# Optimization experiments

Hardware: AMD Instinct MI355X
Metric: run time of the kernel (lower is better)

Reference implementation:

```python
import jax, jax.numpy as jnp
import numpy as np

EPS = 1e-6


def _rmsnorm(x, w):
    var = jnp.mean(x * x, axis=-1, keepdims=True)
    return x * jax.lax.rsqrt(var + EPS) * w


def _rotate_half(x):
    h = x.shape[-1] // 2
    return jnp.concatenate([-x[..., h:], x[..., :h]], axis=-1)


def setup_inputs() -> dict:
    key = jax.random.key(0)
    B, T, H = 2, 2048, 2048
    nh, nkv, d = 16, 8, 128
    max_pos = 4096
    ks = jax.random.split(key, 6)
    s = 0.02
    x = jax.random.normal(ks[0], (B, T, H), jnp.float32)
    # real RoPE tables (Qwen3 uses rope_theta=1e6)
    inv_freq = 1.0 / (1e6 ** (np.arange(0, d, 2, dtype=np.float64) / d))
    freqs = np.outer(np.arange(max_pos), inv_freq)
    emb = np.concatenate([freqs, freqs], axis=-1)
    cos = jnp.asarray(np.cos(emb), jnp.float32)
    sin = jnp.asarray(np.sin(emb), jnp.float32)
    position_ids = jnp.broadcast_to(jnp.arange(T, dtype=jnp.int32)[None, :], (B, T))
    Wq = jax.random.normal(ks[1], (nh * d, H), jnp.float32) * s
    Wk = jax.random.normal(ks[2], (nkv * d, H), jnp.float32) * s
    Wv = jax.random.normal(ks[3], (nkv * d, H), jnp.float32) * s
    Wo = jax.random.normal(ks[4], (H, nh * d), jnp.float32) * s
    q_norm_w = jnp.ones((d,), jnp.float32)
    k_norm_w = jnp.ones((d,), jnp.float32)
    return {"x": x, "cos": cos, "sin": sin, "position_ids": position_ids,
            "Wq": Wq, "Wk": Wk, "Wv": Wv, "Wo": Wo,
            "q_norm_w": q_norm_w, "k_norm_w": k_norm_w}


def reference(x, cos, sin, position_ids, Wq, Wk, Wv, Wo, q_norm_w, k_norm_w):
    B, T, H = x.shape
    d = q_norm_w.shape[0]
    nh = Wq.shape[0] // d
    nkv = Wk.shape[0] // d
    groups = nh // nkv

    # QKV projections (F.linear: x @ W.T)
    q = jnp.einsum('bth,oh->bto', x, Wq).reshape(B, T, nh, d).transpose(0, 2, 1, 3)   # [B,nh,T,d]
    k = jnp.einsum('bth,oh->bto', x, Wk).reshape(B, T, nkv, d).transpose(0, 2, 1, 3)  # [B,nkv,T,d]
    v = jnp.einsum('bth,oh->bto', x, Wv).reshape(B, T, nkv, d).transpose(0, 2, 1, 3)

    # per-head RMSNorm on q and k
    q = _rmsnorm(q, q_norm_w)
    k = _rmsnorm(k, k_norm_w)

    # RoPE
    cos_b = cos[position_ids][:, None, :, :]  # [B,1,T,d]
    sin_b = sin[position_ids][:, None, :, :]
    q = q * cos_b + _rotate_half(q) * sin_b
    k = k * cos_b + _rotate_half(k) * sin_b

    # GQA expand (repeat_interleave along head dim)
    if groups > 1:
        k = jnp.repeat(k, groups, axis=1)
        v = jnp.repeat(v, groups, axis=1)

    # causal SDPA
    scale = 1.0 / jnp.sqrt(jnp.asarray(d, x.dtype))
    scores = jnp.einsum('bhqd,bhkd->bhqk', q, k) * scale  # [B,nh,T,T]
    causal = jnp.tril(jnp.ones((T, T), bool))
    scores = jnp.where(causal[None, None], scores, jnp.asarray(-jnp.inf, scores.dtype))
    probs = jax.nn.softmax(scores, axis=-1)
    attn = jnp.einsum('bhqk,bhkd->bhqd', probs, v)  # [B,nh,T,d]

    attn = attn.transpose(0, 2, 1, 3).reshape(B, T, nh * d)
    return jnp.einsum('bto,ho->bth', attn, Wo)
```

## Files before the change

kernel.cpp:

```cpp
#include <hip/hip_runtime.h>
#include <stdint.h>
#include <stddef.h>

typedef unsigned short u16;
typedef __attribute__((ext_vector_type(4))) unsigned short u16x4;
typedef __attribute__((ext_vector_type(8))) short bf16x8;
typedef __attribute__((ext_vector_type(4))) float f32x4;
typedef __attribute__((ext_vector_type(16))) float f32x16;

#define B_   2
#define T_   2048
#define NH   16
#define NKV  8
#define HD   128

__device__ __forceinline__ u16 f2bf(float f) {
  union { float f; uint32_t u; } v; v.f = f;
  uint32_t u = v.u;
  u += 0x7FFFu + ((u >> 16) & 1u);
  return (u16)(u >> 16);
}
__device__ __forceinline__ float bf2f(u16 h) {
  union { uint32_t u; float f; } v; v.u = ((uint32_t)h) << 16;
  return v.f;
}
__device__ __forceinline__ uint32_t cvt_pk_bf16(float lo, float hi) {
  uint32_t r;
  asm("v_cvt_pk_bf16_f32 %0, %1, %2" : "=v"(r) : "v"(lo), "v"(hi));
  return r;
}

__device__ __forceinline__ void gload_lds16(const void* g, void* l) {
  __builtin_amdgcn_global_load_lds(
      (__attribute__((address_space(1))) void*)g,
      (__attribute__((address_space(3))) void*)l, 16, 0, 0);
}

__global__ __launch_bounds__(256) void cvt_all(const float* __restrict__ x,
                                               const float* __restrict__ Wq,
                                               const float* __restrict__ Wk,
                                               const float* __restrict__ Wv,
                                               const float* __restrict__ Wo,
                                               u16* __restrict__ ws0) {
  const int blk = blockIdx.x;
  const float* src; u16* dst; int lb;
  if (blk < 8192)       { src = x;  dst = ws0;              lb = blk; }
  else if (blk < 12288) { src = Wq; dst = ws0 +  8388608;   lb = blk - 8192; }
  else if (blk < 14336) { src = Wk; dst = ws0 + 12582912;   lb = blk - 12288; }
  else if (blk < 16384) { src = Wv; dst = ws0 + 14680064;   lb = blk - 14336; }
  else                  { src = Wo; dst = ws0 + 16777216;   lb = blk - 16384; }
  const int i = lb * 256 + threadIdx.x;
  float4 v = reinterpret_cast<const float4*>(src)[i];
  u16x4 o;
  o.x = f2bf(v.x); o.y = f2bf(v.y); o.z = f2bf(v.z); o.w = f2bf(v.w);
  reinterpret_cast<u16x4*>(dst)[i] = o;
}

template<int BM, int BN, int STORE>
__global__ __launch_bounds__(512, 2) void gemm2(const u16* __restrict__ A,
                                                const u16* __restrict__ Bm,
                                                void* __restrict__ C0,
                                                void* __restrict__ C1,
                                                void* __restrict__ C2,
                                                int M, int N, int K) {
  constexpr int FM  = BM / 32;
  constexpr int FN  = BN / 64;
  constexpr int ASZ = BM * 64;
  constexpr int BSZ = BN * 64;
  __shared__ u16 lds[2 * (ASZ + BSZ)];

  const int tid  = threadIdx.x;
  const int lane = tid & 63;
  const int wid  = tid >> 6;
  const int lr   = lane & 15;
  const int lg   = lane >> 4;
  const int wm0 = (wid >> 2) * (BM / 2);
  const int wn0 = (wid & 3) * (BN / 4);

  const int s  = ((blockIdx.x & 7) << 5) | (blockIdx.x >> 3);
  const int nx = N / BN;
  const int m0 = (s / nx) * BM;
  const int n0 = (s % nx) * BN;

  f32x4 acc[FM][FN];
#pragma unroll
  for (int i = 0; i < FM; ++i)
#pragma unroll
    for (int j = 0; j < FN; ++j) acc[i][j] = (f32x4){0.f, 0.f, 0.f, 0.f};

  auto stage = [&](int kt, int p) {
    const int k0 = kt << 6;
    u16* Ab = lds + p * (ASZ + BSZ);
    u16* Bb = Ab + ASZ;
#pragma unroll
    for (int it = 0; it < BM / 64; ++it) {
      const int CI = it * 512 + tid;
      const int row = CI >> 3, c = CI & 7;
      gload_lds16(A + (size_t)(m0 + row) * K + k0 + ((c ^ (row & 7)) << 3),
                  (char*)Ab + (size_t)CI * 16);
    }
#pragma unroll
    for (int it = 0; it < BN / 64; ++it) {
      const int CI = it * 512 + tid;
      const int row = CI >> 3, c = CI & 7;
      gload_lds16(Bm + (size_t)(n0 + row) * K + k0 + ((c ^ (row & 7)) << 3),
                  (char*)Bb + (size_t)CI * 16);
    }
  };

  const int nk = K >> 6;
  stage(0, 0);
  __syncthreads();
  int cur = 0;
  for (int kt = 0; kt < nk; ++kt) {
    if (kt + 1 < nk) stage(kt + 1, cur ^ 1);
    const u16* Ab = lds + cur * (ASZ + BSZ);
    const u16* Bb = Ab + ASZ;
#pragma unroll
    for (int kk = 0; kk < 2; ++kk) {
      bf16x8 af[FM], bfr[FN];
#pragma unroll
      for (int mt = 0; mt < FM; ++mt) {
        const int ar = wm0 + mt * 16 + lr;
        af[mt] = *reinterpret_cast<const bf16x8*>(
            (const char*)Ab + ar * 128 + ((kk * 64 + lg * 16) ^ ((ar & 7) << 4)));
      }
#pragma unroll
      for (int nt = 0; nt < FN; ++nt) {
        const int br = wn0 + nt * 16 + lr;
        bfr[nt] = *reinterpret_cast<const bf16x8*>(
            (const char*)Bb + br * 128 + ((kk * 64 + lg * 16) ^ ((br & 7) << 4)));
      }
      __builtin_amdgcn_s_setprio(1);
#pragma unroll
      for (int mt = 0; mt < FM; ++mt)
#pragma unroll
        for (int nt = 0; nt < FN; ++nt)
          acc[mt][nt] = __builtin_amdgcn_mfma_f32_16x16x32_bf16(
              af[mt], bfr[nt], acc[mt][nt], 0, 0, 0);
      __builtin_amdgcn_s_setprio(0);
    }
    __syncthreads();
    cur ^= 1;
  }

  if (STORE == 3) {
    u16* Qd = (u16*)C0; u16* Kd = (u16*)C1; u16* Vd = (u16*)C2;
    if (n0 < 2048) {
#pragma unroll
      for (int mt = 0; mt < FM; ++mt) {
        const int row = m0 + wm0 + mt * 16 + lg * 4;
#pragma unroll
        for (int nt = 0; nt < FN; ++nt) {
          const int col = n0 + wn0 + nt * 16 + lr;
#pragma unroll
          for (int r = 0; r < 4; ++r)
            Qd[(size_t)(row + r) * 2048 + col] = f2bf(acc[mt][nt][r]);
        }
      }
    } else if (n0 < 3072) {
#pragma unroll
      for (int mt = 0; mt < FM; ++mt) {
        const int row = m0 + wm0 + mt * 16 + lg * 4;
#pragma unroll
        for (int nt = 0; nt < FN; ++nt) {
          const int col = n0 + wn0 + nt * 16 + lr - 2048;
#pragma unroll
          for (int r = 0; r < 4; ++r)
            Kd[(size_t)(row + r) * 1024 + col] = f2bf(acc[mt][nt][r]);
        }
      }
    } else {
#pragma unroll
      for (int mt = 0; mt < FM; ++mt) {
        const int row = m0 + wm0 + mt * 16 + lg * 4;
        const int b = row >> 11;
        const int t = row & (T_ - 1);
#pragma unroll
        for (int nt = 0; nt < FN; ++nt) {
          const int vc = n0 + wn0 + nt * 16 + lr - 3072;
          u16x4 v;
          v.x = f2bf(acc[mt][nt][0]); v.y = f2bf(acc[mt][nt][1]);
          v.z = f2bf(acc[mt][nt][2]); v.w = f2bf(acc[mt][nt][3]);
          *reinterpret_cast<u16x4*>(Vd + ((size_t)(b * 1024 + vc)) * T_ + t) = v;
        }
      }
    }
  } else {
    float* C = (float*)C0;
#pragma unroll
    for (int mt = 0; mt < FM; ++mt) {
      const int row = m0 + wm0 + mt * 16 + lg * 4;
#pragma unroll
      for (int nt = 0; nt < FN; ++nt) {
        const int col = n0 + wn0 + nt * 16 + lr;
#pragma unroll
        for (int r = 0; r < 4; ++r)
          C[(size_t)(row + r) * N + col] = acc[mt][nt][r];
      }
    }
  }
}

__global__ __launch_bounds__(256) void rms_rope(u16* __restrict__ Q, u16* __restrict__ Kb,
                                                const float* __restrict__ cosT,
                                                const float* __restrict__ sinT,
                                                const int* __restrict__ pos,
                                                const float* __restrict__ qw,
                                                const float* __restrict__ kw) {
  const int wave = blockIdx.x * 4 + (threadIdx.x >> 6);
  const int lane = threadIdx.x & 63;
  const int bt = wave & (B_ * T_ - 1);
  const int hh = wave >> 12;
  u16* ptr;
  const float* w;
  if (hh < NH) { ptr = Q + (size_t)bt * (NH * HD) + hh * HD; w = qw; }
  else         { ptr = Kb + (size_t)bt * (NKV * HD) + (hh - NH) * HD; w = kw; }
  const int p = pos[bt];

  float e0 = bf2f(ptr[lane]);
  float e1 = bf2f(ptr[lane + 64]);
  float ss = e0 * e0 + e1 * e1;
#pragma unroll
  for (int off = 1; off < 64; off <<= 1) ss += __shfl_xor(ss, off, 64);
  const float r = rsqrtf(ss * (1.0f / 128.0f) + 1e-6f);
  const float n0 = e0 * r * w[lane];
  const float n1 = e1 * r * w[lane + 64];
  const float c0 = cosT[(size_t)p * HD + lane], c1 = cosT[(size_t)p * HD + lane + 64];
  const float s0 = sinT[(size_t)p * HD + lane], s1 = sinT[(size_t)p * HD + lane + 64];
  ptr[lane]      = f2bf(n0 * c0 - n1 * s0);
  ptr[lane + 64] = f2bf(n1 * c1 + n0 * s1);
}

__global__ __launch_bounds__(256, 2) void flash_attn3(const u16* __restrict__ Qw,
                                                      const u16* __restrict__ Kw,
                                                      const u16* __restrict__ VTw,
                                                      u16* __restrict__ Ow) {
  __shared__ __align__(16) char smem[65536];

  const int tid  = threadIdx.x;
  const int lane = tid & 63;
  const int wid  = tid >> 6;
  const int rl   = lane & 31;
  const int hi   = lane >> 5;
  const int blk  = blockIdx.x;
  const int qtr = blk >> 5;
  const int qt  = (blk < 256) ? (15 - qtr) : (qtr - 8);
  const int bh  = blk & 31;
  const int b   = bh >> 4, h = bh & 15, kvh = h >> 1;
  const int q0w = qt * 128 + wid * 32;
  const int qg  = q0w + rl;
  const int swz = (rl & 7) << 4;

  bf16x8 qf[8];
  {
    const u16* qp = Qw + ((size_t)(b * T_) + qg) * (NH * HD) + h * HD + hi * 8;
#pragma unroll
    for (int kd = 0; kd < 8; ++kd) qf[kd] = *reinterpret_cast<const bf16x8*>(qp + kd * 16);
  }

  f32x16 ot[4];
#pragma unroll
  for (int dt = 0; dt < 4; ++dt)
#pragma unroll
    for (int r = 0; r < 16; ++r) ot[dt][r] = 0.f;
  float m = -1e30f, lsum = 0.f;
  const float scale = 0.08838834764831845f;

  auto stageKV = [&](int kt, int p) {
    char* Kb = smem + p * 32768;
    char* Vb = Kb + 16384;
    {
      const int row = tid >> 4, ch = tid & 15;
#pragma unroll
      for (int it = 0; it < 4; ++it) {
        const int rr = it * 16 + row;
        const int scol = ((ch * 16) ^ ((rr & 7) << 4)) >> 1;
        gload_lds16(Kw + ((size_t)(b * T_) + kt * 64 + rr) * (NKV * HD) + kvh * HD + scol,
                    Kb + (it * 256 + tid) * 16);
      }
    }
    {
      const int row = tid >> 3, ch = tid & 7;
#pragma unroll
      for (int it = 0; it < 4; ++it) {
        const int rr = it * 32 + row;
        const int scol = ((ch * 16) ^ ((rr & 7) << 4)) >> 1;
        gload_lds16(VTw + ((size_t)((b * NKV + kvh) * HD) + rr) * T_ + kt * 64 + scol,
                    Vb + (it * 256 + tid) * 16);
      }
    }
  };

  const int nkt = 2 * qt + 2;
  stageKV(0, 0);
  __syncthreads();
  for (int kt = 0; kt < nkt; ++kt) {
    const int cur = kt & 1;
    if (kt + 1 < nkt) stageKV(kt + 1, cur ^ 1);

    if (64 * kt <= q0w + 31) {
      const u16* Kb = (const u16*)(smem + cur * 32768);
      const u16* Vb = (const u16*)(smem + cur * 32768 + 16384);

      f32x16 s0, s1;
#pragma unroll
      for (int r = 0; r < 16; ++r) { s0[r] = 0.f; s1[r] = 0.f; }
      __builtin_amdgcn_s_setprio(1);
#pragma unroll
      for (int kd = 0; kd < 8; ++kd) {
        const int cb = (kd * 32 + hi * 16) ^ swz;
        const bf16x8 k0 = *reinterpret_cast<const bf16x8*>((const char*)Kb + rl * 256 + cb);
        const bf16x8 k1 = *reinterpret_cast<const bf16x8*>((const char*)Kb + (32 + rl) * 256 + cb);
        s0 = __builtin_amdgcn_mfma_f32_32x32x16_bf16(k0, qf[kd], s0, 0, 0, 0);
        s1 = __builtin_amdgcn_mfma_f32_32x32x16_bf16(k1, qf[kd], s1, 0, 0, 0);
      }
      __builtin_amdgcn_s_setprio(0);

      const int kv0 = kt * 64;
      const bool maskT = (kv0 + 63 > q0w);
      float rm = -1e30f;
#pragma unroll
      for (int r = 0; r < 16; ++r) {
        const int cr = (r & 3) + 8 * (r >> 2) + 4 * hi;
        float a = s0[r] * scale, c = s1[r] * scale;
        if (maskT) {
          if (kv0 + cr > qg)      a = -1e30f;
          if (kv0 + 32 + cr > qg) c = -1e30f;
        }
        s0[r] = a; s1[r] = c;
        rm = fmaxf(rm, fmaxf(a, c));
      }
      rm = fmaxf(rm, __shfl_xor(rm, 32));
      const float mn = fmaxf(m, rm);
      const float al = __expf(m - mn);
      m = mn;
      float rs = 0.f;
#pragma unroll
      for (int r = 0; r < 16; ++r) {
        const float p0 = __expf(s0[r] - mn);
        const float p1 = __expf(s1[r] - mn);
        s0[r] = p0; s1[r] = p1;
        rs += p0 + p1;
      }
      rs += __shfl_xor(rs, 32);
      lsum = lsum * al + rs;
#pragma unroll
      for (int dt = 0; dt < 4; ++dt)
#pragma unroll
        for (int r = 0; r < 16; ++r) ot[dt][r] *= al;

      bf16x8 pf[2][2];
#pragma unroll
      for (int ks = 0; ks < 2; ++ks) {
        {
          uint32_t X0 = cvt_pk_bf16(s0[8 * ks + 0], s0[8 * ks + 1]);
          uint32_t X1 = cvt_pk_bf16(s0[8 * ks + 2], s0[8 * ks + 3]);
          uint32_t Y0 = cvt_pk_bf16(s0[8 * ks + 4], s0[8 * ks + 5]);
          uint32_t Y1 = cvt_pk_bf16(s0[8 * ks + 6], s0[8 * ks + 7]);
          asm volatile("v_permlane32_swap_b32 %0, %1" : "+v"(X0), "+v"(Y0));
          asm volatile("v_permlane32_swap_b32 %0, %1" : "+v"(X1), "+v"(Y1));
          union { uint32_t w[4]; bf16x8 v; } u;
          u.w[0] = X0; u.w[1] = X1; u.w[2] = Y0; u.w[3] = Y1;
          pf[0][ks] = u.v;
        }
        {
          uint32_t X0 = cvt_pk_bf16(s1[8 * ks + 0], s1[8 * ks + 1]);
          uint32_t X1 = cvt_pk_bf16(s1[8 * ks + 2], s1[8 * ks + 3]);
          uint32_t Y0 = cvt_pk_bf16(s1[8 * ks + 4], s1[8 * ks + 5]);
          uint32_t Y1 = cvt_pk_bf16(s1[8 * ks + 6], s1[8 * ks + 7]);
          asm volatile("v_permlane32_swap_b32 %0, %1" : "+v"(X0), "+v"(Y0));
          asm volatile("v_permlane32_swap_b32 %0, %1" : "+v"(X1), "+v"(Y1));
          union { uint32_t w[4]; bf16x8 v; } u;
          u.w[0] = X0; u.w[1] = X1; u.w[2] = Y0; u.w[3] = Y1;
          pf[1][ks] = u.v;
        }
      }

      __builtin_amdgcn_s_setprio(1);
#pragma unroll
      for (int dt = 0; dt < 4; ++dt) {
        const int rv = dt * 32 + rl;
#pragma unroll
        for (int kvc = 0; kvc < 2; ++kvc)
#pragma unroll
          for (int ks = 0; ks < 2; ++ks) {
            const int cb = (kvc * 64 + ks * 32 + hi * 16) ^ ((rv & 7) << 4);
            const bf16x8 vf = *reinterpret_cast<const bf16x8*>((const char*)Vb + rv * 128 + cb);
            ot[dt] = __builtin_amdgcn_mfma_f32_32x32x16_bf16(vf, pf[kvc][ks], ot[dt], 0, 0, 0);
          }
      }
      __builtin_amdgcn_s_setprio(0);
    }
    __syncthreads();
  }

  const float inv = 1.0f / lsum;
  u16* ep = (u16*)smem + wid * (32 * 136);
#pragma unroll
  for (int dt = 0; dt < 4; ++dt)
#pragma unroll
    for (int r = 0; r < 16; ++r) {
      const int d = dt * 32 + (r & 3) + 8 * (r >> 2) + 4 * hi;
      ep[rl * 136 + d] = f2bf(ot[dt][r] * inv);
    }
  const int dh = hi * 64;
  const u16* srcp = (u16*)smem + wid * (32 * 136) + rl * 136 + dh;
  u16* gdst = Ow + ((size_t)(b * T_) + q0w + rl) * (NH * HD) + h * HD + dh;
#pragma unroll
  for (int c2 = 0; c2 < 8; ++c2)
    *reinterpret_cast<bf16x8*>(gdst + c2 * 8) =
        *reinterpret_cast<const bf16x8*>(srcp + c2 * 8);
}

extern "C" void kernel_launch(void* const* d_in, const int* in_sizes, int n_in,
                              void* d_out, int out_size, void* d_ws, size_t ws_size,
                              hipStream_t stream) {
  (void)in_sizes; (void)n_in; (void)out_size; (void)ws_size;
  const float* x    = (const float*)d_in[0];
  const float* cosT = (const float*)d_in[1];
  const float* sinT = (const float*)d_in[2];
  const int*   pos  = (const int*)d_in[3];
  const float* Wq   = (const float*)d_in[4];
  const float* Wk   = (const float*)d_in[5];
  const float* Wv   = (const float*)d_in[6];
  const float* Wo   = (const float*)d_in[7];
  const float* qw   = (const float*)d_in[8];
  const float* kw   = (const float*)d_in[9];
  float* out = (float*)d_out;

  char* ws = (char*)d_ws;
  u16* xb   = (u16*)(ws + 0);
  u16* Wqb  = (u16*)(ws + 16777216);
  u16* Qws  = (u16*)(ws + 41943040);
  u16* Kws  = (u16*)(ws + 58720256);
  u16* VTws = (u16*)(ws + 67108864);
  u16* Aws  = (u16*)(ws + 75497472);
  u16* Wob  = (u16*)(ws + 33554432);

  cvt_all<<<20480, 256, 0, stream>>>(x, Wq, Wk, Wv, Wo, (u16*)ws);

  gemm2<256, 256, 3><<<256, 512, 0, stream>>>(xb, Wqb, Qws, Kws, VTws,
                                              4096, 4096, 2048);

  rms_rope<<<24576, 256, 0, stream>>>(Qws, Kws, cosT, sinT, pos, qw, kw);

  flash_attn3<<<512, 256, 0, stream>>>(Qws, Kws, VTws, Aws);

  gemm2<128, 256, 2><<<256, 512, 0, stream>>>(Aws, Wob, out, nullptr, nullptr,
                                              4096, 2048, 2048);
}
```

Before: 200.4 us.

## Fold softmax scale into Q, use exp2, lazy rescale, wider K swizzle

Folds the 1/sqrt(d)*log2(e) factor into Q during the RMSNorm/RoPE pass, so the attention kernel uses raw v_exp_f32 (exp2) with no per-score scaling. The output rescale is skipped unless the running max grows by more than 8 (in log2 units) anywhere in the wave. Mask work is moved outside the per-element loop for unmasked tiles. The K LDS swizzle is widened to 16 rows to reduce bank conflicts. The lazy rescale adds a wave-wide vote and allows unnormalised values up to 2^8 in the accumulators, and storing the scaled Q in bf16 slightly changes rounding.

```diff
diff --git a/kernel.cpp b/kernel.cpp
--- a/kernel.cpp
+++ b/kernel.cpp
@@ -14,6 +14,8 @@
 #define NKV  8
 #define HD   128
 
+#define QSCALE 0.1275174457f
+
 __device__ __forceinline__ u16 f2bf(float f) {
   union { float f; uint32_t u; } v; v.f = f;
   uint32_t u = v.u;
@@ -27,6 +29,11 @@
 __device__ __forceinline__ uint32_t cvt_pk_bf16(float lo, float hi) {
   uint32_t r;
   asm("v_cvt_pk_bf16_f32 %0, %1, %2" : "=v"(r) : "v"(lo), "v"(hi));
+  return r;
+}
+__device__ __forceinline__ float fexp2(float x) {
+  float r;
+  asm("v_exp_f32 %0, %1" : "=v"(r) : "v"(x));
   return r;
 }
 
@@ -214,8 +221,9 @@
   const int hh = wave >> 12;
   u16* ptr;
   const float* w;
-  if (hh < NH) { ptr = Q + (size_t)bt * (NH * HD) + hh * HD; w = qw; }
-  else         { ptr = Kb + (size_t)bt * (NKV * HD) + (hh - NH) * HD; w = kw; }
+  float post;
+  if (hh < NH) { ptr = Q + (size_t)bt * (NH * HD) + hh * HD; w = qw; post = QSCALE; }
+  else         { ptr = Kb + (size_t)bt * (NKV * HD) + (hh - NH) * HD; w = kw; post = 1.0f; }
   const int p = pos[bt];
 
   float e0 = bf2f(ptr[lane]);
@@ -223,7 +231,7 @@
   float ss = e0 * e0 + e1 * e1;
 #pragma unroll
   for (int off = 1; off < 64; off <<= 1) ss += __shfl_xor(ss, off, 64);
-  const float r = rsqrtf(ss * (1.0f / 128.0f) + 1e-6f);
+  const float r = rsqrtf(ss * (1.0f / 128.0f) + 1e-6f) * post;
   const float n0 = e0 * r * w[lane];
   const float n1 = e1 * r * w[lane + 64];
   const float c0 = cosT[(size_t)p * HD + lane], c1 = cosT[(size_t)p * HD + lane + 64];
@@ -232,7 +240,7 @@
   ptr[lane + 64] = f2bf(n1 * c1 + n0 * s1);
 }
 
-__global__ __launch_bounds__(256, 2) void flash_attn3(const u16* __restrict__ Qw,
+__global__ __launch_bounds__(256, 2) void flash_attn5(const u16* __restrict__ Qw,
                                                       const u16* __restrict__ Kw,
                                                       const u16* __restrict__ VTw,
                                                       u16* __restrict__ Ow) {
@@ -250,7 +258,8 @@
   const int b   = bh >> 4, h = bh & 15, kvh = h >> 1;
   const int q0w = qt * 128 + wid * 32;
   const int qg  = q0w + rl;
-  const int swz = (rl & 7) << 4;
+  const int kswz = (rl & 15) << 4;
+  const int vswz = (rl & 7) << 4;
 
   bf16x8 qf[8];
   {
@@ -265,7 +274,6 @@
 #pragma unroll
     for (int r = 0; r < 16; ++r) ot[dt][r] = 0.f;
   float m = -1e30f, lsum = 0.f;
-  const float scale = 0.08838834764831845f;
 
   auto stageKV = [&](int kt, int p) {
     char* Kb = smem + p * 32768;
@@ -275,7 +283,7 @@
 #pragma unroll
       for (int it = 0; it < 4; ++it) {
         const int rr = it * 16 + row;
-        const int scol = ((ch * 16) ^ ((rr & 7) << 4)) >> 1;
+        const int scol = ((ch * 16) ^ ((rr & 15) << 4)) >> 1;
         gload_lds16(Kw + ((size_t)(b * T_) + kt * 64 + rr) * (NKV * HD) + kvh * HD + scol,
                     Kb + (it * 256 + tid) * 16);
       }
@@ -309,7 +317,7 @@
       __builtin_amdgcn_s_setprio(1);
 #pragma unroll
       for (int kd = 0; kd < 8; ++kd) {
-        const int cb = (kd * 32 + hi * 16) ^ swz;
+        const int cb = (kd * 32 + hi * 16) ^ kswz;
         const bf16x8 k0 = *reinterpret_cast<const bf16x8*>((const char*)Kb + rl * 256 + cb);
         const bf16x8 k1 = *reinterpret_cast<const bf16x8*>((const char*)Kb + (32 + rl) * 256 + cb);
         s0 = __builtin_amdgcn_mfma_f32_32x32x16_bf16(k0, qf[kd], s0, 0, 0, 0);
@@ -320,35 +328,42 @@
       const int kv0 = kt * 64;
       const bool maskT = (kv0 + 63 > q0w);
       float rm = -1e30f;
-#pragma unroll
-      for (int r = 0; r < 16; ++r) {
-        const int cr = (r & 3) + 8 * (r >> 2) + 4 * hi;
-        float a = s0[r] * scale, c = s1[r] * scale;
-        if (maskT) {
+      if (maskT) {
+#pragma unroll
+        for (int r = 0; r < 16; ++r) {
+          const int cr = (r & 3) + 8 * (r >> 2) + 4 * hi;
+          float a = s0[r], c = s1[r];
           if (kv0 + cr > qg)      a = -1e30f;
           if (kv0 + 32 + cr > qg) c = -1e30f;
-        }
-        s0[r] = a; s1[r] = c;
-        rm = fmaxf(rm, fmaxf(a, c));
+          s0[r] = a; s1[r] = c;
+          rm = fmaxf(rm, fmaxf(a, c));
+        }
+      } else {
+#pragma unroll
+        for (int r = 0; r < 16; ++r) rm = fmaxf(rm, fmaxf(s0[r], s1[r]));
       }
       rm = fmaxf(rm, __shfl_xor(rm, 32));
-      const float mn = fmaxf(m, rm);
-      const float al = __expf(m - mn);
-      m = mn;
+
+      if (!__all(rm <= m + 8.0f)) {
+        const float mn = fmaxf(m, rm);
+        const float al = fexp2(m - mn);
+        lsum *= al;
+#pragma unroll
+        for (int dt = 0; dt < 4; ++dt)
+#pragma unroll
+          for (int r = 0; r < 16; ++r) ot[dt][r] *= al;
+        m = mn;
+      }
       float rs = 0.f;
 #pragma unroll
       for (int r = 0; r < 16; ++r) {
-        const float p0 = __expf(s0[r] - mn);
-        const float p1 = __expf(s1[r] - mn);
+        const float p0 = fexp2(s0[r] - m);
+        const float p1 = fexp2(s1[r] - m);
         s0[r] = p0; s1[r] = p1;
         rs += p0 + p1;
       }
       rs += __shfl_xor(rs, 32);
-      lsum = lsum * al + rs;
-#pragma unroll
-      for (int dt = 0; dt < 4; ++dt)
-#pragma unroll
-        for (int r = 0; r < 16; ++r) ot[dt][r] *= al;
+      lsum += rs;
 
       bf16x8 pf[2][2];
 #pragma unroll
@@ -432,11 +447,11 @@
   char* ws = (char*)d_ws;
   u16* xb   = (u16*)(ws + 0);
   u16* Wqb  = (u16*)(ws + 16777216);
+  u16* Wob  = (u16*)(ws + 33554432);
   u16* Qws  = (u16*)(ws + 41943040);
   u16* Kws  = (u16*)(ws + 58720256);
   u16* VTws = (u16*)(ws + 67108864);
   u16* Aws  = (u16*)(ws + 75497472);
-  u16* Wob  = (u16*)(ws + 33554432);
 
   cvt_all<<<20480, 256, 0, stream>>>(x, Wq, Wk, Wv, Wo, (u16*)ws);
 
@@ -445,7 +460,7 @@
 
   rms_rope<<<24576, 256, 0, stream>>>(Qws, Kws, cosT, sinT, pos, qw, kw);
 
-  flash_attn3<<<512, 256, 0, stream>>>(Qws, Kws, VTws, Aws);
+  flash_attn5<<<512, 256, 0, stream>>>(Qws, Kws, VTws, Aws);
 
   gemm2<128, 256, 2><<<256, 512, 0, stream>>>(Aws, Wob, out, nullptr, nullptr,
                                               4096, 2048, 2048);
```

New measurement: 191.5 us. 1.05x faster.
